# Kernel tuning notes

Hardware: AMD Instinct MI355X
Metric: run time of the kernel (lower is better)

Reference implementation:

```python
import jax, jax.numpy as jnp
import numpy as np

POS_TH = 0.5
NEG_TH = 0.4
NEGPOS_RATIO = 3
BBOX_ALPHA = 1.5
CONF_ALPHA = 1.0
VAR_CXCY = 0.1
VAR_WH = 0.2
NUM_CLASSES = 41
B, P, G = 8, 100000, 16


def setup_inputs() -> dict:
    key = jax.random.key(0)
    k = jax.random.split(key, 8)
    loc_data = jax.random.normal(k[0], (B, P, 4), dtype=jnp.float32)
    conf_data = jax.random.normal(k[1], (B, P, NUM_CLASSES), dtype=jnp.float32)
    # priors in (cx, cy, w, h), normalized coords
    p_cxy = jax.random.uniform(k[2], (P, 2), minval=0.0, maxval=1.0)
    p_wh = jax.random.uniform(k[3], (P, 2), minval=0.02, maxval=0.3)
    priors = jnp.concatenate([p_cxy, p_wh], axis=1).astype(jnp.float32)
    # gt boxes in point form (x1, y1, x2, y2)
    g_cxy = jax.random.uniform(k[4], (B, G, 2), minval=0.15, maxval=0.85)
    g_wh = jax.random.uniform(k[5], (B, G, 2), minval=0.05, maxval=0.4)
    gt_boxes = jnp.concatenate([
        jnp.clip(g_cxy - g_wh / 2, 0.0, 1.0),
        jnp.clip(g_cxy + g_wh / 2, 0.0, 1.0),
    ], axis=-1).astype(jnp.float32)
    gt_labels = jax.random.randint(k[6], (B, G), 1, NUM_CLASSES)
    return {"loc_data": loc_data, "conf_data": conf_data, "priors": priors,
            "gt_boxes": gt_boxes, "gt_labels": gt_labels}


def point_form(pr):
    return jnp.concatenate([pr[:, :2] - pr[:, 2:] / 2,
                            pr[:, :2] + pr[:, 2:] / 2], axis=1)


def jaccard(a, b):
    # a: [G,4] xyxy, b: [P,4] xyxy -> [G,P]
    lt = jnp.maximum(a[:, None, :2], b[None, :, :2])
    rb = jnp.minimum(a[:, None, 2:], b[None, :, 2:])
    wh = jnp.clip(rb - lt, 0.0)
    inter = wh[..., 0] * wh[..., 1]
    area_a = ((a[:, 2] - a[:, 0]) * (a[:, 3] - a[:, 1]))[:, None]
    area_b = ((b[:, 2] - b[:, 0]) * (b[:, 3] - b[:, 1]))[None, :]
    return inter / (area_a + area_b - inter)


def encode(matched, priors):
    # matched [P,4] xyxy, priors [P,4] cxcywh -> SSD offsets with variances
    g_cxcy = ((matched[:, :2] + matched[:, 2:]) / 2 - priors[:, :2]) / (VAR_CXCY * priors[:, 2:])
    g_wh = jnp.log(jnp.clip((matched[:, 2:] - matched[:, :2]) / priors[:, 2:], 1e-8)) / VAR_WH
    return jnp.concatenate([g_cxcy, g_wh], axis=1)


def match_one(gt_box, gt_label, priors):
    # gt_box [G,4], gt_label [G], priors [P,4] -> loc_t [P,4], conf_t [P]
    pf = point_form(priors)
    ov = jaccard(gt_box, pf)                      # [G,P]
    best_truth_ov = ov.max(axis=0)                # [P]
    best_truth_idx = ov.argmax(axis=0)            # [P]
    best_prior_idx = ov.argmax(axis=1)            # [G] best prior per gt
    # force-match each gt to its best prior
    best_truth_ov = best_truth_ov.at[best_prior_idx].set(2.0)
    best_truth_idx = best_truth_idx.at[best_prior_idx].set(jnp.arange(gt_box.shape[0]))
    conf = gt_label[best_truth_idx]
    conf = jnp.where(best_truth_ov < POS_TH, -1, conf)   # neutral
    conf = jnp.where(best_truth_ov < NEG_TH, 0, conf)    # background
    loc = encode(gt_box[best_truth_idx], priors)
    return loc, conf


def reference(loc_data, conf_data, priors, gt_boxes, gt_labels):
    bsz, n_pri, n_cls = conf_data.shape
    loc_t, conf_t = jax.vmap(match_one, in_axes=(0, 0, None))(gt_boxes, gt_labels, priors)
    pos = conf_t > 0                               # [B,P]
    num_pos = pos.sum(axis=1)                      # [B]
    # pos_weights: uniform 1/num_pos per image (ones split then normalized)
    pos_w = pos.astype(loc_data.dtype) / jnp.clip(num_pos, 1).astype(loc_data.dtype)[:, None]
    # localization: weighted SmoothL1 over positives
    d = loc_data - loc_t
    sl1 = jnp.where(jnp.abs(d) < 1.0, 0.5 * d * d, jnp.abs(d) - 0.5)
    loss_B = (pos_w[..., None] * sl1).sum() * BBOX_ALPHA
    # OHEM hard negative mining on background-suppression loss
    loss_c = jax.nn.logsumexp(conf_data, axis=-1) - conf_data[..., 0]
    loss_c = jnp.where(pos | (conf_t < 0), 0.0, loss_c)
    order = jnp.argsort(-loss_c, axis=1)
    rank = jnp.argsort(order, axis=1)
    num_neg = jnp.clip(NEGPOS_RATIO * num_pos, 0, n_pri - 1)
    neg = (rank < num_neg[:, None]) & (~pos) & (conf_t >= 0)
    keep = (pos | neg).astype(conf_data.dtype)
    logp = jax.nn.log_softmax(conf_data, axis=-1)
    ce = -jnp.take_along_axis(logp, jnp.clip(conf_t, 0)[..., None], axis=-1)[..., 0]
    total_pos = jnp.clip(num_pos.sum(), 1).astype(conf_data.dtype)
    loss_C = (ce * keep).sum() * CONF_ALPHA / total_pos
    return (loss_B + loss_C) / bsz
```

## Files before the change

kernel.cpp:

```cpp
#include <hip/hip_runtime.h>
#include <stdint.h>

#define BATCH 8
#define NPRI 100000
#define NGT 16
#define NCLS 41
#define F_POS_TH 0.5f
#define F_NEG_TH 0.4f

static constexpr int TPB = 256;
static constexpr int MCHUNK = 16;
static constexpr int MLEN = (NPRI + MCHUNK - 1) / MCHUNK;

static constexpr int WTPB = 64;
static constexpr int CPT = WTPB * NCLS / 4;
static constexpr int BLK_PER_B = 224;
static constexpr int TILES_PER_B = (NPRI + WTPB - 1) / WTPB;
static constexpr int H0BIN = 256;
static constexpr int NBIN = 4096;

static constexpr size_t OFF_KEY  = 0;
static constexpr size_t OFF_GTC  = OFF_KEY + (size_t)BATCH*NPRI*4;
static constexpr size_t OFF_HG   = OFF_GTC + BATCH*NGT*8;
static constexpr size_t OFF_NPOS = OFF_HG + (size_t)BATCH*H0BIN*4;
static constexpr size_t OFF_SL1  = OFF_NPOS + BATCH*4;
static constexpr size_t OFF_CEP  = OFF_SL1  + BATCH*4;
static constexpr size_t OFF_NEG  = OFF_CEP  + BATCH*4;
static constexpr size_t OFF_FTK  = OFF_NEG  + BATCH*4;
static constexpr int ZERO_U32 = (int)((OFF_FTK + 4 - OFF_HG) / 4);

__device__ inline float smoothl1(float d) {
  float a = fabsf(d);
  return a < 1.f ? 0.5f * d * d : a - 0.5f;
}
__device__ inline float aload_f32(const float* p) {
  return __hip_atomic_load(p, __ATOMIC_RELAXED, __HIP_MEMORY_SCOPE_AGENT);
}
__device__ __forceinline__ void gll16(const void* gsrc, void* ldst) {
  __builtin_amdgcn_global_load_lds(
      (const __attribute__((address_space(1))) void*)gsrc,
      (__attribute__((address_space(3))) void*)ldst, 16, 0, 0);
}

__global__ void k_init(unsigned* __restrict__ z, unsigned long long* __restrict__ gtc) {
  int t = threadIdx.x;
  for (int i = t; i < ZERO_U32; i += 512) z[i] = 0u;
  if (t < BATCH * NGT) gtc[t] = 0xFFFFFFFFull;
}

__global__ __launch_bounds__(TPB) void k_match(const float* __restrict__ priors,
                                               const float* __restrict__ gtb,
                                               unsigned long long* __restrict__ gtc) {
  int bg = blockIdx.y;
  int t = threadIdx.x;
  const float4 gv = ((const float4*)gtb)[bg];
  float garea = (gv.z - gv.x) * (gv.w - gv.y);
  int pend = min(NPRI, (int)(blockIdx.x + 1) * MLEN);
  unsigned long long best = 0;
  for (int p = blockIdx.x * MLEN + t; p < pend; p += TPB) {
    float4 pv = ((const float4*)priors)[p];
    float px1 = pv.x - 0.5f * pv.z, py1 = pv.y - 0.5f * pv.w;
    float px2 = pv.x + 0.5f * pv.z, py2 = pv.y + 0.5f * pv.w;
    float ix = fmaxf(fminf(px2, gv.z) - fmaxf(px1, gv.x), 0.f);
    float iy = fmaxf(fminf(py2, gv.w) - fmaxf(py1, gv.y), 0.f);
    float inter = ix * iy;
    float parea = (px2 - px1) * (py2 - py1);
    float iou = inter / (parea + garea - inter);
    unsigned long long comp = ((unsigned long long)__float_as_uint(iou) << 32)
                            | (unsigned long long)(0xFFFFFFFFu - (unsigned)p);
    best = best > comp ? best : comp;
  }
#pragma unroll
  for (int off = 32; off; off >>= 1) {
    unsigned long long o = (unsigned long long)__shfl_xor((long long)best, off, 64);
    best = best > o ? best : o;
  }
  __shared__ unsigned long long red[4];
  if ((t & 63) == 0) red[t >> 6] = best;
  __syncthreads();
  if (t == 0) {
    unsigned long long r = red[0];
    r = r > red[1] ? r : red[1];
    r = r > red[2] ? r : red[2];
    r = r > red[3] ? r : red[3];
    atomicMax(&gtc[bg], r);
  }
}

__global__ __launch_bounds__(WTPB) void k_conf(
    const float* __restrict__ loc, const float* __restrict__ conf,
    const float* __restrict__ priors, const float* __restrict__ gtb,
    const int* __restrict__ gtl, const unsigned long long* __restrict__ gtc,
    unsigned* __restrict__ key, unsigned* __restrict__ histg,
    unsigned* __restrict__ npos, float* __restrict__ sl1sum, float* __restrict__ cepos) {
  __shared__ float buf[2][CPT * 4];
  __shared__ unsigned hcb[H0BIN];
  int t = threadIdx.x;
  int b = blockIdx.x / BLK_PER_B;
  int sub = blockIdx.x % BLK_PER_B;
  const float4* conf4 = (const float4*)conf;
  const size_t bbase4 = (size_t)b * NPRI * NCLS / 4;
  const size_t maxc4 = (size_t)BATCH * NPRI * NCLS / 4 - 1;
  float acc_s = 0.f, acc_c = 0.f; unsigned acc_p = 0;
#pragma unroll
  for (int u = 0; u < H0BIN / WTPB; u++) hcb[t + u * WTPB] = 0u;

  {
    size_t base4 = bbase4 + (size_t)sub * CPT;
#pragma unroll
    for (int u = 0; u < 10; u++) {
      size_t g4 = base4 + (unsigned)(t + u * WTPB);
      if (g4 > maxc4) g4 = maxc4;
      gll16(conf4 + g4, &buf[0][(t + u * WTPB) * 4]);
    }
    if (t < CPT - 10 * WTPB) {
      size_t g4 = base4 + (unsigned)(t + 10 * WTPB);
      if (g4 > maxc4) g4 = maxc4;
      gll16(conf4 + g4, &buf[0][(t + 10 * WTPB) * 4]);
    }
  }
  int cur = 0;
  for (int tidx = sub; tidx < TILES_PER_B; tidx += BLK_PER_B) {
    int p = tidx * WTPB + t;
    bool valid = p < NPRI;
    int pc = valid ? p : NPRI - 1;
    float4 pv = ((const float4*)priors)[pc];
    float4 ld = ((const float4*)loc)[(size_t)b * NPRI + pc];
    int nxt = tidx + BLK_PER_B;
    if (nxt < TILES_PER_B) {
      size_t base4 = bbase4 + (size_t)nxt * CPT;
#pragma unroll
      for (int u = 0; u < 10; u++) {
        size_t g4 = base4 + (unsigned)(t + u * WTPB);
        if (g4 > maxc4) g4 = maxc4;
        gll16(conf4 + g4, &buf[cur ^ 1][(t + u * WTPB) * 4]);
      }
      if (t < CPT - 10 * WTPB) {
        size_t g4 = base4 + (unsigned)(t + 10 * WTPB);
        if (g4 > maxc4) g4 = maxc4;
        gll16(conf4 + g4, &buf[cur ^ 1][(t + 10 * WTPB) * 4]);
      }
      asm volatile("s_waitcnt vmcnt(11)" ::: "memory");
    } else {
      asm volatile("s_waitcnt vmcnt(0)" ::: "memory");
    }
    __builtin_amdgcn_sched_barrier(0);
    unsigned kkreg = 0u;
    if (valid) {
      float px1 = pv.x - 0.5f * pv.z, py1 = pv.y - 0.5f * pv.w;
      float px2 = pv.x + 0.5f * pv.z, py2 = pv.y + 0.5f * pv.w;
      float parea = (px2 - px1) * (py2 - py1);
      float bov = 0.f; int g = 0;
#pragma unroll
      for (int gg = 0; gg < NGT; gg++) {
        const float4 gv = ((const float4*)gtb)[b * NGT + gg];
        float ix = fmaxf(fminf(px2, gv.z) - fmaxf(px1, gv.x), 0.f);
        float iy = fmaxf(fminf(py2, gv.w) - fmaxf(py1, gv.y), 0.f);
        float inter = ix * iy;
        float garea = (gv.z - gv.x) * (gv.w - gv.y);
        float iou = inter / (parea + garea - inter);
        if (iou > bov) { bov = iou; g = gg; }
      }
      float o = bov;
#pragma unroll
      for (int gg = 0; gg < NGT; gg++) {
        unsigned long long c64 = gtc[b * NGT + gg];
        unsigned pw = 0xFFFFFFFFu - (unsigned)(c64 & 0xFFFFFFFFull);
        if ((unsigned)p == pw) { o = 2.0f; g = gg; }
      }
      int c = gtl[b * NGT + g];
      if (o < F_POS_TH) c = -1;
      if (o < F_NEG_TH) c = 0;
      const float* r = &buf[cur][t * NCLS];
      float s = 0.f, r0 = 0.f, rc = 0.f;
#pragma unroll
      for (int j = 0; j < NCLS; j++) {
        float v = r[j];
        s += __expf(v);
        if (j == 0) r0 = v;
        if (j == c) rc = v;
      }
      float lse = __logf(s);
      kkreg = (c == 0) ? __float_as_uint(lse - r0) : 0u;
      key[(size_t)b * NPRI + p] = kkreg;
      atomicAdd(&hcb[kkreg >> 24], 1u);
      if (c > 0) {
        acc_p += 1;
        acc_c += lse - rc;
        const float4 gvb = ((const float4*)gtb)[b * NGT + g];
        float tx = ((gvb.x + gvb.z) * 0.5f - pv.x) / (0.1f * pv.z);
        float ty = ((gvb.y + gvb.w) * 0.5f - pv.y) / (0.1f * pv.w);
        float tw = __logf(fmaxf((gvb.z - gvb.x) / pv.z, 1e-8f)) / 0.2f;
        float th = __logf(fmaxf((gvb.w - gvb.y) / pv.w, 1e-8f)) / 0.2f;
        acc_s += smoothl1(ld.x - tx) + smoothl1(ld.y - ty)
               + smoothl1(ld.z - tw) + smoothl1(ld.w - th);
      }
    }
    cur ^= 1;
  }
#pragma unroll
  for (int u = 0; u < H0BIN / WTPB; u++) {
    unsigned v = hcb[t + u * WTPB];
    if (v) atomicAdd(&histg[b * H0BIN + t + u * WTPB], v);
  }
  float vs = acc_s, vc = acc_c; unsigned vp = acc_p;
#pragma unroll
  for (int off = 32; off; off >>= 1) {
    vs += __shfl_down(vs, off, 64);
    vc += __shfl_down(vc, off, 64);
    vp += __shfl_down(vp, off, 64);
  }
  if (t == 0) {
    if (vp) atomicAdd(&npos[b], vp);
    if (vs != 0.f) atomicAdd(&sl1sum[b], vs);
    if (vc != 0.f) atomicAdd(&cepos[b], vc);
  }
}

__global__ __launch_bounds__(1024) void k_select(
    const unsigned* __restrict__ key, const unsigned* __restrict__ histg,
    const unsigned* __restrict__ npos, const float* __restrict__ sl1sum,
    const float* __restrict__ cepos, float* __restrict__ negsum,
    unsigned* __restrict__ final_tk, float* __restrict__ out) {
  __shared__ unsigned hc[NBIN];
  __shared__ unsigned pcs[256], sc[256];
  __shared__ int wA; __shared__ unsigned kexA;
  __shared__ unsigned kS, prefS;
  __shared__ float redf[16];
  int b = blockIdx.x, t = threadIdx.x;
  unsigned k0 = min(3u * npos[b], (unsigned)(NPRI - 1));
  const int iters = (NPRI + 1023) / 1024;
  if (t < 256) { unsigned v = histg[b * H0BIN + t]; pcs[t] = v; sc[t] = v; }
  if (t == 0) { kS = 0u; prefS = 0u; wA = -1; }
  __syncthreads();
  for (int off = 1; off < 256; off <<= 1) {
    unsigned v = 0;
    if (t < 256) v = (t + off < 256) ? sc[t + off] : 0u;
    __syncthreads();
    if (t < 256) sc[t] += v;
    __syncthreads();
  }
  if (t < 256) {
    unsigned excl = sc[t] - pcs[t];
    if (k0 > 0 && excl < k0 && k0 <= excl + pcs[t]) { wA = t; kexA = excl; }
  }
  __syncthreads();
  if (t == 0 && wA >= 0) { prefS = ((unsigned)wA) << 24; kS = k0 - kexA; }
  __syncthreads();
  for (int lvl = 1; lvl <= 2; lvl++) {
    unsigned k = kS;
    int shift = (lvl == 1) ? 12 : 0;
    int lowcut = (lvl == 1) ? 24 : 12;
    for (int i = t; i < NBIN; i += 1024) hc[i] = 0u;
    if (t == 0) wA = -1;
    __syncthreads();
    unsigned pre = prefS >> lowcut;
    if (k > 0) {
      for (int n = 0; n < iters; n++) {
        int i = n * 1024 + t;
        if (i < NPRI) {
          unsigned kk = key[(size_t)b * NPRI + i];
          if ((kk >> lowcut) == pre) atomicAdd(&hc[(kk >> shift) & 0xFFFu], 1u);
        }
      }
    }
    __syncthreads();
    if (t < 256) {
      unsigned cs = 0;
#pragma unroll
      for (int u = 0; u < 16; u++) cs += hc[t * 16 + u];
      pcs[t] = cs; sc[t] = cs;
    }
    __syncthreads();
    for (int off = 1; off < 256; off <<= 1) {
      unsigned v = 0;
      if (t < 256) v = (t + off < 256) ? sc[t + off] : 0u;
      __syncthreads();
      if (t < 256) sc[t] += v;
      __syncthreads();
    }
    if (t < 256) {
      unsigned excl = sc[t] - pcs[t];
      if (k > 0 && excl < k && k <= excl + pcs[t]) { wA = t; kexA = excl; }
    }
    __syncthreads();
    if (wA >= 0 && t < 64) {
      int w = wA; unsigned exw = kexA;
      unsigned v = (t < 16) ? hc[w * 16 + t] : 0u;
      unsigned sufv = v;
#pragma unroll
      for (int off = 1; off < 16; off <<= 1) {
        unsigned x = __shfl_down(sufv, off, 64);
        if (t + off < 16) sufv += x;
      }
      unsigned excl2 = exw + (sufv - v);
      if (t < 16 && excl2 < k && k <= excl2 + v) {
        prefS |= ((unsigned)(w * 16 + t)) << shift;
        kS = k - excl2;
      }
    }
    __syncthreads();
  }
  unsigned Tu = prefS;
  unsigned tie = kS;
  float acc = 0.f;
  if (k0 > 0) {
    for (int n = 0; n < iters; n++) {
      int i = n * 1024 + t;
      if (i < NPRI) {
        unsigned kk = key[(size_t)b * NPRI + i];
        if (kk > Tu) acc += __uint_as_float(kk);
      }
    }
  }
#pragma unroll
  for (int off = 32; off; off >>= 1) acc += __shfl_down(acc, off, 64);
  if ((t & 63) == 0) redf[t >> 6] = acc;
  __syncthreads();
  if (t == 0) {
    float tot = 0.f;
    for (int wv = 0; wv < 16; wv++) tot += redf[wv];
    if (k0 > 0) tot += (float)tie * __uint_as_float(Tu);
    negsum[b] = tot;
    __threadfence();
    unsigned r2 = atomicAdd(final_tk, 1u);
    if (r2 == BATCH - 1) {
      __threadfence();
      float lb = 0.f, ctot = 0.f; unsigned tp = 0;
      for (int bb = 0; bb < BATCH; bb++) {
        lb += aload_f32(&sl1sum[bb]) / fmaxf((float)npos[bb], 1.f);
        tp += npos[bb];
        ctot += aload_f32(&cepos[bb]) + aload_f32(&negsum[bb]);
      }
      out[0] = (1.5f * lb + ctot / fmaxf((float)tp, 1.f)) / (float)BATCH;
      *final_tk = 0;
    }
  }
}

extern "C" void kernel_launch(void* const* d_in, const int* in_sizes, int n_in,
                              void* d_out, int out_size, void* d_ws, size_t ws_size,
                              hipStream_t stream) {
  const float* loc = (const float*)d_in[0];
  const float* conf = (const float*)d_in[1];
  const float* priors = (const float*)d_in[2];
  const float* gtb = (const float*)d_in[3];
  const int* gtl = (const int*)d_in[4];
  char* ws = (char*)d_ws;
  unsigned* key = (unsigned*)(ws + OFF_KEY);
  unsigned long long* gtc = (unsigned long long*)(ws + OFF_GTC);
  unsigned* histg = (unsigned*)(ws + OFF_HG);
  unsigned* npos = (unsigned*)(ws + OFF_NPOS);
  float* sl1sum = (float*)(ws + OFF_SL1);
  float* cepos = (float*)(ws + OFF_CEP);
  float* negsum = (float*)(ws + OFF_NEG);
  unsigned* final_tk = (unsigned*)(ws + OFF_FTK);
  float* out = (float*)d_out;

  k_init<<<1, 512, 0, stream>>>(histg, gtc);
  dim3 gridM(MCHUNK, BATCH * NGT);
  k_match<<<gridM, TPB, 0, stream>>>(priors, gtb, gtc);
  k_conf<<<BATCH * BLK_PER_B, WTPB, 0, stream>>>(loc, conf, priors, gtb, gtl, gtc,
                                                 key, histg, npos, sl1sum, cepos);
  k_select<<<BATCH, 1024, 0, stream>>>(key, histg, npos, sl1sum, cepos,
                                       negsum, final_tk, out);
}
```

Measured before the change: 151.3 us.

## Replace LDS double-buffered conf loads with coalesced register loads and shared atomic row sums

The persistent 64-thread double-buffered global_load_lds pipeline in k_conf is replaced by a one-tile-per-wave grid of 256-thread blocks. Each lane loads 11 coalesced float4 chunks straight into registers, exponentiates them, and accumulates per-prior exp sums into shared memory with atomics split at row boundaries. The positive-class logit is then re-read from global memory, and per-block reductions go through shared memory. This trades the explicit prefetch pipeline for more occupancy and parallelism, at the cost of many LDS atomics and a much larger grid.

```diff
diff --git a/kernel.cpp b/kernel.cpp
--- a/kernel.cpp
+++ b/kernel.cpp
@@ -12,10 +12,9 @@
 static constexpr int MCHUNK = 16;
 static constexpr int MLEN = (NPRI + MCHUNK - 1) / MCHUNK;
 
-static constexpr int WTPB = 64;
-static constexpr int CPT = WTPB * NCLS / 4;
-static constexpr int BLK_PER_B = 224;
-static constexpr int TILES_PER_B = (NPRI + WTPB - 1) / WTPB;
+static constexpr int TILES_PER_B = (NPRI + 63) / 64;
+static constexpr int CBLK = (TILES_PER_B + 3) / 4;
+static constexpr int CW = 64 * NCLS / 4;
 static constexpr int H0BIN = 256;
 static constexpr int NBIN = 4096;
 
@@ -29,17 +28,14 @@
 static constexpr size_t OFF_FTK  = OFF_NEG  + BATCH*4;
 static constexpr int ZERO_U32 = (int)((OFF_FTK + 4 - OFF_HG) / 4);
 
+typedef float f32x4 __attribute__((ext_vector_type(4)));
+
 __device__ inline float smoothl1(float d) {
   float a = fabsf(d);
   return a < 1.f ? 0.5f * d * d : a - 0.5f;
 }
 __device__ inline float aload_f32(const float* p) {
   return __hip_atomic_load(p, __ATOMIC_RELAXED, __HIP_MEMORY_SCOPE_AGENT);
-}
-__device__ __forceinline__ void gll16(const void* gsrc, void* ldst) {
-  __builtin_amdgcn_global_load_lds(
-      (const __attribute__((address_space(1))) void*)gsrc,
-      (__attribute__((address_space(3))) void*)ldst, 16, 0, 0);
 }
 
 __global__ void k_init(unsigned* __restrict__ z, unsigned long long* __restrict__ gtc) {
@@ -53,16 +49,16 @@
                                                unsigned long long* __restrict__ gtc) {
   int bg = blockIdx.y;
   int t = threadIdx.x;
-  const float4 gv = ((const float4*)gtb)[bg];
-  float garea = (gv.z - gv.x) * (gv.w - gv.y);
+  const f32x4 gv = ((const f32x4*)gtb)[bg];
+  float garea = (gv[2] - gv[0]) * (gv[3] - gv[1]);
   int pend = min(NPRI, (int)(blockIdx.x + 1) * MLEN);
   unsigned long long best = 0;
   for (int p = blockIdx.x * MLEN + t; p < pend; p += TPB) {
-    float4 pv = ((const float4*)priors)[p];
-    float px1 = pv.x - 0.5f * pv.z, py1 = pv.y - 0.5f * pv.w;
-    float px2 = pv.x + 0.5f * pv.z, py2 = pv.y + 0.5f * pv.w;
-    float ix = fmaxf(fminf(px2, gv.z) - fmaxf(px1, gv.x), 0.f);
-    float iy = fmaxf(fminf(py2, gv.w) - fmaxf(py1, gv.y), 0.f);
+    f32x4 pv = ((const f32x4*)priors)[p];
+    float px1 = pv[0] - 0.5f * pv[2], py1 = pv[1] - 0.5f * pv[3];
+    float px2 = pv[0] + 0.5f * pv[2], py2 = pv[1] + 0.5f * pv[3];
+    float ix = fmaxf(fminf(px2, gv[2]) - fmaxf(px1, gv[0]), 0.f);
+    float iy = fmaxf(fminf(py2, gv[3]) - fmaxf(py1, gv[1]), 0.f);
     float inter = ix * iy;
     float parea = (px2 - px1) * (py2 - py1);
     float iou = inter / (parea + garea - inter);
@@ -87,77 +83,78 @@
   }
 }
 
-__global__ __launch_bounds__(WTPB) void k_conf(
+__global__ __launch_bounds__(256, 4) void k_conf(
     const float* __restrict__ loc, const float* __restrict__ conf,
     const float* __restrict__ priors, const float* __restrict__ gtb,
     const int* __restrict__ gtl, const unsigned long long* __restrict__ gtc,
     unsigned* __restrict__ key, unsigned* __restrict__ histg,
     unsigned* __restrict__ npos, float* __restrict__ sl1sum, float* __restrict__ cepos) {
-  __shared__ float buf[2][CPT * 4];
+  __shared__ float sums[4][64];
+  __shared__ float r0s[4][64];
   __shared__ unsigned hcb[H0BIN];
-  int t = threadIdx.x;
-  int b = blockIdx.x / BLK_PER_B;
-  int sub = blockIdx.x % BLK_PER_B;
-  const float4* conf4 = (const float4*)conf;
-  const size_t bbase4 = (size_t)b * NPRI * NCLS / 4;
-  const size_t maxc4 = (size_t)BATCH * NPRI * NCLS / 4 - 1;
-  float acc_s = 0.f, acc_c = 0.f; unsigned acc_p = 0;
-#pragma unroll
-  for (int u = 0; u < H0BIN / WTPB; u++) hcb[t + u * WTPB] = 0u;
-
-  {
-    size_t base4 = bbase4 + (size_t)sub * CPT;
-#pragma unroll
-    for (int u = 0; u < 10; u++) {
-      size_t g4 = base4 + (unsigned)(t + u * WTPB);
-      if (g4 > maxc4) g4 = maxc4;
-      gll16(conf4 + g4, &buf[0][(t + u * WTPB) * 4]);
-    }
-    if (t < CPT - 10 * WTPB) {
-      size_t g4 = base4 + (unsigned)(t + 10 * WTPB);
-      if (g4 > maxc4) g4 = maxc4;
-      gll16(conf4 + g4, &buf[0][(t + 10 * WTPB) * 4]);
-    }
-  }
-  int cur = 0;
-  for (int tidx = sub; tidx < TILES_PER_B; tidx += BLK_PER_B) {
-    int p = tidx * WTPB + t;
-    bool valid = p < NPRI;
-    int pc = valid ? p : NPRI - 1;
-    float4 pv = ((const float4*)priors)[pc];
-    float4 ld = ((const float4*)loc)[(size_t)b * NPRI + pc];
-    int nxt = tidx + BLK_PER_B;
-    if (nxt < TILES_PER_B) {
-      size_t base4 = bbase4 + (size_t)nxt * CPT;
-#pragma unroll
-      for (int u = 0; u < 10; u++) {
-        size_t g4 = base4 + (unsigned)(t + u * WTPB);
-        if (g4 > maxc4) g4 = maxc4;
-        gll16(conf4 + g4, &buf[cur ^ 1][(t + u * WTPB) * 4]);
-      }
-      if (t < CPT - 10 * WTPB) {
-        size_t g4 = base4 + (unsigned)(t + 10 * WTPB);
-        if (g4 > maxc4) g4 = maxc4;
-        gll16(conf4 + g4, &buf[cur ^ 1][(t + 10 * WTPB) * 4]);
-      }
-      asm volatile("s_waitcnt vmcnt(11)" ::: "memory");
-    } else {
-      asm volatile("s_waitcnt vmcnt(0)" ::: "memory");
-    }
-    __builtin_amdgcn_sched_barrier(0);
-    unsigned kkreg = 0u;
+  __shared__ float redS[4], redC[4]; __shared__ unsigned redP[4];
+  const int t = threadIdx.x, w = t >> 6, l = t & 63;
+  const int b = blockIdx.y;
+  const int tile = blockIdx.x * 4 + w;
+  hcb[t] = 0u;
+  sums[w][l] = 0.f;
+  __syncthreads();
+  float accS = 0.f, accC = 0.f; unsigned accP = 0;
+  if (tile < TILES_PER_B) {
+    const f32x4* c4 = (const f32x4*)conf;
+    const size_t base = (size_t)b * (NPRI * NCLS / 4) + (size_t)tile * CW;
+    const size_t bend = (size_t)(b + 1) * (NPRI * NCLS / 4) - 1;
+    f32x4 rr[11];
+#pragma unroll
+    for (int u = 0; u < 11; u++) {
+      size_t ix = base + (unsigned)(u * 64 + l);
+      if (ix > bend) ix = bend;
+      rr[u] = c4[ix];
+    }
+    const int p = tile * 64 + l;
+    const bool valid = p < NPRI;
+    const int pc = valid ? p : NPRI - 1;
+    const f32x4 pv = ((const f32x4*)priors)[pc];
+    const f32x4 ld = ((const f32x4*)loc)[(size_t)b * NPRI + pc];
+#pragma unroll
+    for (int u = 0; u < 11; u++) {
+      int cidx = u * 64 + l;
+      if (cidx < CW) {
+        int f = cidx * 4;
+        int r0 = (int)((unsigned)f / 41u);
+        int rem = f - r0 * 41;
+        float e0 = __expf(rr[u][0]);
+        float e1 = __expf(rr[u][1]);
+        float e2 = __expf(rr[u][2]);
+        float e3 = __expf(rr[u][3]);
+        int nlo = 41 - rem;
+        float slo = e0, shi = 0.f;
+        if (nlo > 1) slo += e1; else shi += e1;
+        if (nlo > 2) slo += e2; else shi += e2;
+        if (nlo > 3) slo += e3; else shi += e3;
+        atomicAdd(&sums[w][r0], slo);
+        if (nlo <= 3) atomicAdd(&sums[w][r0 + 1], shi);
+        if (rem == 0) r0s[w][r0] = rr[u][0];
+        else if (nlo <= 3) {
+          float v = (nlo == 1) ? rr[u][1] : (nlo == 2) ? rr[u][2] : rr[u][3];
+          r0s[w][r0 + 1] = v;
+        }
+      }
+    }
+    float lse = __logf(sums[w][l]);
+    float r0v = r0s[w][l];
     if (valid) {
-      float px1 = pv.x - 0.5f * pv.z, py1 = pv.y - 0.5f * pv.w;
-      float px2 = pv.x + 0.5f * pv.z, py2 = pv.y + 0.5f * pv.w;
+      float px1 = pv[0] - 0.5f * pv[2], py1 = pv[1] - 0.5f * pv[3];
+      float px2 = pv[0] + 0.5f * pv[2], py2 = pv[1] + 0.5f * pv[3];
       float parea = (px2 - px1) * (py2 - py1);
       float bov = 0.f; int g = 0;
 #pragma unroll
       for (int gg = 0; gg < NGT; gg++) {
-        const float4 gv = ((const float4*)gtb)[b * NGT + gg];
-        float ix = fmaxf(fminf(px2, gv.z) - fmaxf(px1, gv.x), 0.f);
-        float iy = fmaxf(fminf(py2, gv.w) - fmaxf(py1, gv.y), 0.f);
+        const f32x4 gv = ((const f32x4*)gtb)[b * NGT + gg];
+        float ix = fmaxf(fminf(px2, gv[2]) - fmaxf(px1, gv[0]), 0.f);
+        float iy = fmaxf(fminf(py2, gv[3]) - fmaxf(py1, gv[1]), 0.f);
         float inter = ix * iy;
-        float garea = (gv.z - gv.x) * (gv.w - gv.y);
+        float garea = (gv[2] - gv[0]) * (gv[3] - gv[1]);
         float iou = inter / (parea + garea - inter);
         if (iou > bov) { bov = iou; g = gg; }
       }
@@ -171,49 +168,41 @@
       int c = gtl[b * NGT + g];
       if (o < F_POS_TH) c = -1;
       if (o < F_NEG_TH) c = 0;
-      const float* r = &buf[cur][t * NCLS];
-      float s = 0.f, r0 = 0.f, rc = 0.f;
-#pragma unroll
-      for (int j = 0; j < NCLS; j++) {
-        float v = r[j];
-        s += __expf(v);
-        if (j == 0) r0 = v;
-        if (j == c) rc = v;
-      }
-      float lse = __logf(s);
-      kkreg = (c == 0) ? __float_as_uint(lse - r0) : 0u;
+      unsigned kkreg = (c == 0) ? __float_as_uint(lse - r0v) : 0u;
       key[(size_t)b * NPRI + p] = kkreg;
       atomicAdd(&hcb[kkreg >> 24], 1u);
       if (c > 0) {
-        acc_p += 1;
-        acc_c += lse - rc;
-        const float4 gvb = ((const float4*)gtb)[b * NGT + g];
-        float tx = ((gvb.x + gvb.z) * 0.5f - pv.x) / (0.1f * pv.z);
-        float ty = ((gvb.y + gvb.w) * 0.5f - pv.y) / (0.1f * pv.w);
-        float tw = __logf(fmaxf((gvb.z - gvb.x) / pv.z, 1e-8f)) / 0.2f;
-        float th = __logf(fmaxf((gvb.w - gvb.y) / pv.w, 1e-8f)) / 0.2f;
-        acc_s += smoothl1(ld.x - tx) + smoothl1(ld.y - ty)
-               + smoothl1(ld.z - tw) + smoothl1(ld.w - th);
-      }
-    }
-    cur ^= 1;
-  }
-#pragma unroll
-  for (int u = 0; u < H0BIN / WTPB; u++) {
-    unsigned v = hcb[t + u * WTPB];
-    if (v) atomicAdd(&histg[b * H0BIN + t + u * WTPB], v);
-  }
-  float vs = acc_s, vc = acc_c; unsigned vp = acc_p;
+        accP = 1;
+        float rc = conf[((size_t)b * NPRI + p) * NCLS + c];
+        accC = lse - rc;
+        const f32x4 gvb = ((const f32x4*)gtb)[b * NGT + g];
+        float tx = ((gvb[0] + gvb[2]) * 0.5f - pv[0]) / (0.1f * pv[2]);
+        float ty = ((gvb[1] + gvb[3]) * 0.5f - pv[1]) / (0.1f * pv[3]);
+        float tw = __logf(fmaxf((gvb[2] - gvb[0]) / pv[2], 1e-8f)) / 0.2f;
+        float th = __logf(fmaxf((gvb[3] - gvb[1]) / pv[3], 1e-8f)) / 0.2f;
+        accS = smoothl1(ld[0] - tx) + smoothl1(ld[1] - ty)
+             + smoothl1(ld[2] - tw) + smoothl1(ld[3] - th);
+      }
+    }
+  }
+  __syncthreads();
+  { unsigned v = hcb[t]; if (v) atomicAdd(&histg[b * H0BIN + t], v); }
+  float vs = accS, vc = accC; unsigned vp = accP;
 #pragma unroll
   for (int off = 32; off; off >>= 1) {
     vs += __shfl_down(vs, off, 64);
     vc += __shfl_down(vc, off, 64);
     vp += __shfl_down(vp, off, 64);
   }
+  if (l == 0) { redS[w] = vs; redC[w] = vc; redP[w] = vp; }
+  __syncthreads();
   if (t == 0) {
-    if (vp) atomicAdd(&npos[b], vp);
-    if (vs != 0.f) atomicAdd(&sl1sum[b], vs);
-    if (vc != 0.f) atomicAdd(&cepos[b], vc);
+    float ts = redS[0] + redS[1] + redS[2] + redS[3];
+    float tc = redC[0] + redC[1] + redC[2] + redC[3];
+    unsigned tp = redP[0] + redP[1] + redP[2] + redP[3];
+    if (tp) atomicAdd(&npos[b], tp);
+    if (ts != 0.f) atomicAdd(&sl1sum[b], ts);
+    if (tc != 0.f) atomicAdd(&cepos[b], tc);
   }
 }
 
@@ -360,8 +349,9 @@
   k_init<<<1, 512, 0, stream>>>(histg, gtc);
   dim3 gridM(MCHUNK, BATCH * NGT);
   k_match<<<gridM, TPB, 0, stream>>>(priors, gtb, gtc);
-  k_conf<<<BATCH * BLK_PER_B, WTPB, 0, stream>>>(loc, conf, priors, gtb, gtl, gtc,
-                                                 key, histg, npos, sl1sum, cepos);
+  dim3 gridC(CBLK, BATCH);
+  k_conf<<<gridC, 256, 0, stream>>>(loc, conf, priors, gtb, gtl, gtc,
+                                    key, histg, npos, sl1sum, cepos);
   k_select<<<BATCH, 1024, 0, stream>>>(key, histg, npos, sl1sum, cepos,
                                        negsum, final_tk, out);
 }
```

Result: slower. 187.0 us (+23.6%).

## Fuse best-prior matching into conf pass and patch forced matches in select

Applied to the files above, without the earlier changes.

Removes the separate k_match kernel. The per-GT best-prior argmax is now computed inside k_conf through LDS atomicMax on packed (iou, index) keys, then merged globally. Because the forced assignment is only known after k_conf finishes, k_select corrects the 16 forced priors per image afterwards: it adjusts the key, the histogram, npos, the SmoothL1 sum and the positive CE sum. It also replaces the most common per-thread histogram atomics (zero keys and bin 0x40) with wave-ballot aggregated adds. The cost is a serial correction step in thread 0, extra LDS atomics in the hot loop, and delicate logic for duplicate forced matches.

```diff
diff --git a/kernel.cpp b/kernel.cpp
--- a/kernel.cpp
+++ b/kernel.cpp
@@ -7,10 +7,6 @@
 #define NCLS 41
 #define F_POS_TH 0.5f
 #define F_NEG_TH 0.4f
-
-static constexpr int TPB = 256;
-static constexpr int MCHUNK = 16;
-static constexpr int MLEN = (NPRI + MCHUNK - 1) / MCHUNK;
 
 static constexpr int WTPB = 64;
 static constexpr int CPT = WTPB * NCLS / 4;
@@ -29,11 +25,24 @@
 static constexpr size_t OFF_FTK  = OFF_NEG  + BATCH*4;
 static constexpr int ZERO_U32 = (int)((OFF_FTK + 4 - OFF_HG) / 4);
 
+typedef float f32x4 __attribute__((ext_vector_type(4)));
+
 __device__ inline float smoothl1(float d) {
   float a = fabsf(d);
   return a < 1.f ? 0.5f * d * d : a - 0.5f;
 }
+__device__ inline float sl1_terms(f32x4 pv, f32x4 ld, f32x4 gv) {
+  float tx = ((gv[0] + gv[2]) * 0.5f - pv[0]) / (0.1f * pv[2]);
+  float ty = ((gv[1] + gv[3]) * 0.5f - pv[1]) / (0.1f * pv[3]);
+  float tw = __logf(fmaxf((gv[2] - gv[0]) / pv[2], 1e-8f)) / 0.2f;
+  float th = __logf(fmaxf((gv[3] - gv[1]) / pv[3], 1e-8f)) / 0.2f;
+  return smoothl1(ld[0] - tx) + smoothl1(ld[1] - ty)
+       + smoothl1(ld[2] - tw) + smoothl1(ld[3] - th);
+}
 __device__ inline float aload_f32(const float* p) {
+  return __hip_atomic_load(p, __ATOMIC_RELAXED, __HIP_MEMORY_SCOPE_AGENT);
+}
+__device__ inline unsigned aload_u32(const unsigned* p) {
   return __hip_atomic_load(p, __ATOMIC_RELAXED, __HIP_MEMORY_SCOPE_AGENT);
 }
 __device__ __forceinline__ void gll16(const void* gsrc, void* ldst) {
@@ -48,62 +57,26 @@
   if (t < BATCH * NGT) gtc[t] = 0xFFFFFFFFull;
 }
 
-__global__ __launch_bounds__(TPB) void k_match(const float* __restrict__ priors,
-                                               const float* __restrict__ gtb,
-                                               unsigned long long* __restrict__ gtc) {
-  int bg = blockIdx.y;
-  int t = threadIdx.x;
-  const float4 gv = ((const float4*)gtb)[bg];
-  float garea = (gv.z - gv.x) * (gv.w - gv.y);
-  int pend = min(NPRI, (int)(blockIdx.x + 1) * MLEN);
-  unsigned long long best = 0;
-  for (int p = blockIdx.x * MLEN + t; p < pend; p += TPB) {
-    float4 pv = ((const float4*)priors)[p];
-    float px1 = pv.x - 0.5f * pv.z, py1 = pv.y - 0.5f * pv.w;
-    float px2 = pv.x + 0.5f * pv.z, py2 = pv.y + 0.5f * pv.w;
-    float ix = fmaxf(fminf(px2, gv.z) - fmaxf(px1, gv.x), 0.f);
-    float iy = fmaxf(fminf(py2, gv.w) - fmaxf(py1, gv.y), 0.f);
-    float inter = ix * iy;
-    float parea = (px2 - px1) * (py2 - py1);
-    float iou = inter / (parea + garea - inter);
-    unsigned long long comp = ((unsigned long long)__float_as_uint(iou) << 32)
-                            | (unsigned long long)(0xFFFFFFFFu - (unsigned)p);
-    best = best > comp ? best : comp;
-  }
-#pragma unroll
-  for (int off = 32; off; off >>= 1) {
-    unsigned long long o = (unsigned long long)__shfl_xor((long long)best, off, 64);
-    best = best > o ? best : o;
-  }
-  __shared__ unsigned long long red[4];
-  if ((t & 63) == 0) red[t >> 6] = best;
-  __syncthreads();
-  if (t == 0) {
-    unsigned long long r = red[0];
-    r = r > red[1] ? r : red[1];
-    r = r > red[2] ? r : red[2];
-    r = r > red[3] ? r : red[3];
-    atomicMax(&gtc[bg], r);
-  }
-}
-
 __global__ __launch_bounds__(WTPB) void k_conf(
     const float* __restrict__ loc, const float* __restrict__ conf,
     const float* __restrict__ priors, const float* __restrict__ gtb,
-    const int* __restrict__ gtl, const unsigned long long* __restrict__ gtc,
+    const int* __restrict__ gtl,
     unsigned* __restrict__ key, unsigned* __restrict__ histg,
+    unsigned long long* __restrict__ gtc,
     unsigned* __restrict__ npos, float* __restrict__ sl1sum, float* __restrict__ cepos) {
   __shared__ float buf[2][CPT * 4];
   __shared__ unsigned hcb[H0BIN];
+  __shared__ unsigned long long best[NGT];
   int t = threadIdx.x;
   int b = blockIdx.x / BLK_PER_B;
   int sub = blockIdx.x % BLK_PER_B;
-  const float4* conf4 = (const float4*)conf;
+  const f32x4* conf4 = (const f32x4*)conf;
   const size_t bbase4 = (size_t)b * NPRI * NCLS / 4;
   const size_t maxc4 = (size_t)BATCH * NPRI * NCLS / 4 - 1;
   float acc_s = 0.f, acc_c = 0.f; unsigned acc_p = 0;
 #pragma unroll
   for (int u = 0; u < H0BIN / WTPB; u++) hcb[t + u * WTPB] = 0u;
+  if (t < NGT) best[t] = 0;
 
   {
     size_t base4 = bbase4 + (size_t)sub * CPT;
@@ -124,8 +97,8 @@
     int p = tidx * WTPB + t;
     bool valid = p < NPRI;
     int pc = valid ? p : NPRI - 1;
-    float4 pv = ((const float4*)priors)[pc];
-    float4 ld = ((const float4*)loc)[(size_t)b * NPRI + pc];
+    f32x4 pv = ((const f32x4*)priors)[pc];
+    f32x4 ld = ((const f32x4*)loc)[(size_t)b * NPRI + pc];
     int nxt = tidx + BLK_PER_B;
     if (nxt < TILES_PER_B) {
       size_t base4 = bbase4 + (size_t)nxt * CPT;
@@ -147,30 +120,28 @@
     __builtin_amdgcn_sched_barrier(0);
     unsigned kkreg = 0u;
     if (valid) {
-      float px1 = pv.x - 0.5f * pv.z, py1 = pv.y - 0.5f * pv.w;
-      float px2 = pv.x + 0.5f * pv.z, py2 = pv.y + 0.5f * pv.w;
+      float px1 = pv[0] - 0.5f * pv[2], py1 = pv[1] - 0.5f * pv[3];
+      float px2 = pv[0] + 0.5f * pv[2], py2 = pv[1] + 0.5f * pv[3];
       float parea = (px2 - px1) * (py2 - py1);
       float bov = 0.f; int g = 0;
 #pragma unroll
       for (int gg = 0; gg < NGT; gg++) {
-        const float4 gv = ((const float4*)gtb)[b * NGT + gg];
-        float ix = fmaxf(fminf(px2, gv.z) - fmaxf(px1, gv.x), 0.f);
-        float iy = fmaxf(fminf(py2, gv.w) - fmaxf(py1, gv.y), 0.f);
+        const f32x4 gv = ((const f32x4*)gtb)[b * NGT + gg];
+        float ix = fmaxf(fminf(px2, gv[2]) - fmaxf(px1, gv[0]), 0.f);
+        float iy = fmaxf(fminf(py2, gv[3]) - fmaxf(py1, gv[1]), 0.f);
         float inter = ix * iy;
-        float garea = (gv.z - gv.x) * (gv.w - gv.y);
+        float garea = (gv[2] - gv[0]) * (gv[3] - gv[1]);
         float iou = inter / (parea + garea - inter);
         if (iou > bov) { bov = iou; g = gg; }
-      }
-      float o = bov;
-#pragma unroll
-      for (int gg = 0; gg < NGT; gg++) {
-        unsigned long long c64 = gtc[b * NGT + gg];
-        unsigned pw = 0xFFFFFFFFu - (unsigned)(c64 & 0xFFFFFFFFull);
-        if ((unsigned)p == pw) { o = 2.0f; g = gg; }
+        if (iou > 0.f) {
+          unsigned long long comp = ((unsigned long long)__float_as_uint(iou) << 32)
+                                  | (unsigned long long)(0xFFFFFFFFu - (unsigned)p);
+          if (comp > best[gg]) atomicMax(&best[gg], comp);
+        }
       }
       int c = gtl[b * NGT + g];
-      if (o < F_POS_TH) c = -1;
-      if (o < F_NEG_TH) c = 0;
+      if (bov < F_POS_TH) c = -1;
+      if (bov < F_NEG_TH) c = 0;
       const float* r = &buf[cur][t * NCLS];
       float s = 0.f, r0 = 0.f, rc = 0.f;
 #pragma unroll
@@ -183,21 +154,24 @@
       float lse = __logf(s);
       kkreg = (c == 0) ? __float_as_uint(lse - r0) : 0u;
       key[(size_t)b * NPRI + p] = kkreg;
-      atomicAdd(&hcb[kkreg >> 24], 1u);
       if (c > 0) {
         acc_p += 1;
         acc_c += lse - rc;
-        const float4 gvb = ((const float4*)gtb)[b * NGT + g];
-        float tx = ((gvb.x + gvb.z) * 0.5f - pv.x) / (0.1f * pv.z);
-        float ty = ((gvb.y + gvb.w) * 0.5f - pv.y) / (0.1f * pv.w);
-        float tw = __logf(fmaxf((gvb.z - gvb.x) / pv.z, 1e-8f)) / 0.2f;
-        float th = __logf(fmaxf((gvb.w - gvb.y) / pv.w, 1e-8f)) / 0.2f;
-        acc_s += smoothl1(ld.x - tx) + smoothl1(ld.y - ty)
-               + smoothl1(ld.z - tw) + smoothl1(ld.w - th);
-      }
-    }
+        const f32x4 gvb = ((const f32x4*)gtb)[b * NGT + g];
+        acc_s += sl1_terms(pv, ld, gvb);
+      }
+    }
+    unsigned bin = kkreg >> 24;
+    unsigned long long m40 = __ballot(valid && kkreg != 0u && bin == 0x40u);
+    unsigned long long m00 = __ballot(valid && kkreg == 0u);
+    if (m40 && t == __ffsll((long long)m40) - 1)
+      atomicAdd(&hcb[0x40], (unsigned)__popcll(m40));
+    if (m00 && t == __ffsll((long long)m00) - 1)
+      atomicAdd(&hcb[0], (unsigned)__popcll(m00));
+    if (valid && kkreg != 0u && bin != 0x40u) atomicAdd(&hcb[bin], 1u);
     cur ^= 1;
   }
+  if (t < NGT && best[t] != 0) atomicMax(&gtc[b * NGT + t], best[t]);
 #pragma unroll
   for (int u = 0; u < H0BIN / WTPB; u++) {
     unsigned v = hcb[t + u * WTPB];
@@ -218,20 +192,86 @@
 }
 
 __global__ __launch_bounds__(1024) void k_select(
-    const unsigned* __restrict__ key, const unsigned* __restrict__ histg,
-    const unsigned* __restrict__ npos, const float* __restrict__ sl1sum,
-    const float* __restrict__ cepos, float* __restrict__ negsum,
+    const float* __restrict__ loc, const float* __restrict__ conf,
+    const float* __restrict__ priors, const float* __restrict__ gtb,
+    const int* __restrict__ gtl, const unsigned long long* __restrict__ gtc,
+    unsigned* __restrict__ key, const unsigned* __restrict__ histg,
+    unsigned* __restrict__ npos, float* __restrict__ sl1sum,
+    float* __restrict__ cepos, float* __restrict__ negsum,
     unsigned* __restrict__ final_tk, float* __restrict__ out) {
   __shared__ unsigned hc[NBIN];
+  __shared__ unsigned h0s[H0BIN];
   __shared__ unsigned pcs[256], sc[256];
   __shared__ int wA; __shared__ unsigned kexA;
   __shared__ unsigned kS, prefS;
   __shared__ float redf[16];
+  __shared__ unsigned pw16[NGT]; __shared__ float lse16[NGT], bov16[NGT];
+  __shared__ int bidx16[NGT];
   int b = blockIdx.x, t = threadIdx.x;
+  if (t < H0BIN) h0s[t] = histg[b * H0BIN + t];
+  if (t < NGT) {
+    unsigned long long c64 = gtc[b * NGT + t];
+    unsigned p = 0xFFFFFFFFu - (unsigned)(c64 & 0xFFFFFFFFull);
+    pw16[t] = p;
+    const float* row = conf + ((size_t)b * NPRI + p) * NCLS;
+    float s = 0.f;
+    for (int j = 0; j < NCLS; j++) s += __expf(row[j]);
+    lse16[t] = __logf(s);
+    f32x4 pv = ((const f32x4*)priors)[p];
+    float px1 = pv[0] - 0.5f * pv[2], py1 = pv[1] - 0.5f * pv[3];
+    float px2 = pv[0] + 0.5f * pv[2], py2 = pv[1] + 0.5f * pv[3];
+    float parea = (px2 - px1) * (py2 - py1);
+    float bov = 0.f; int g = 0;
+    for (int gg = 0; gg < NGT; gg++) {
+      const f32x4 gv = ((const f32x4*)gtb)[b * NGT + gg];
+      float ix = fmaxf(fminf(px2, gv[2]) - fmaxf(px1, gv[0]), 0.f);
+      float iy = fmaxf(fminf(py2, gv[3]) - fmaxf(py1, gv[1]), 0.f);
+      float inter = ix * iy;
+      float garea = (gv[2] - gv[0]) * (gv[3] - gv[1]);
+      float iou = inter / (parea + garea - inter);
+      if (iou > bov) { bov = iou; g = gg; }
+    }
+    bov16[t] = bov; bidx16[t] = g;
+  }
+  __syncthreads();
+  if (t == 0) {
+    unsigned np = npos[b];
+    float sl = sl1sum[b], cpv = cepos[b];
+    for (int i = 0; i < NGT; i++) {
+      unsigned p = pw16[i];
+      int prev = -1;
+      for (int j = 0; j < i; j++) if (pw16[j] == p) prev = j;
+      float lse = lse16[i];
+      const float* row = conf + ((size_t)b * NPRI + p) * NCLS;
+      f32x4 pv = ((const f32x4*)priors)[p];
+      f32x4 ldv = ((const f32x4*)loc)[(size_t)b * NPRI + p];
+      float newce = lse - row[gtl[b * NGT + i]];
+      float newsl = sl1_terms(pv, ldv, ((const f32x4*)gtb)[b * NGT + i]);
+      if (prev < 0) {
+        float o = bov16[i]; int gold = bidx16[i];
+        int cold = (o < F_NEG_TH) ? 0 : ((o < F_POS_TH) ? -1 : gtl[b * NGT + gold]);
+        if (cold == 0) {
+          unsigned ko = key[(size_t)b * NPRI + p];
+          h0s[ko >> 24] -= 1u; h0s[0] += 1u;
+        } else if (cold > 0) {
+          np -= 1; cpv -= lse - row[cold];
+          sl -= sl1_terms(pv, ldv, ((const f32x4*)gtb)[b * NGT + gold]);
+        }
+        np += 1; cpv += newce; sl += newsl;
+        key[(size_t)b * NPRI + p] = 0u;
+      } else {
+        cpv -= lse - row[gtl[b * NGT + prev]];
+        sl -= sl1_terms(pv, ldv, ((const f32x4*)gtb)[b * NGT + prev]);
+        cpv += newce; sl += newsl;
+      }
+    }
+    npos[b] = np; sl1sum[b] = sl; cepos[b] = cpv;
+    kS = 0u; prefS = 0u; wA = -1;
+  }
+  __syncthreads();
   unsigned k0 = min(3u * npos[b], (unsigned)(NPRI - 1));
   const int iters = (NPRI + 1023) / 1024;
-  if (t < 256) { unsigned v = histg[b * H0BIN + t]; pcs[t] = v; sc[t] = v; }
-  if (t == 0) { kS = 0u; prefS = 0u; wA = -1; }
+  if (t < 256) { unsigned v = h0s[t]; pcs[t] = v; sc[t] = v; }
   __syncthreads();
   for (int off = 1; off < 256; off <<= 1) {
     unsigned v = 0;
@@ -328,8 +368,9 @@
       __threadfence();
       float lb = 0.f, ctot = 0.f; unsigned tp = 0;
       for (int bb = 0; bb < BATCH; bb++) {
-        lb += aload_f32(&sl1sum[bb]) / fmaxf((float)npos[bb], 1.f);
-        tp += npos[bb];
+        unsigned nb = aload_u32(&npos[bb]);
+        lb += aload_f32(&sl1sum[bb]) / fmaxf((float)nb, 1.f);
+        tp += nb;
         ctot += aload_f32(&cepos[bb]) + aload_f32(&negsum[bb]);
       }
       out[0] = (1.5f * lb + ctot / fmaxf((float)tp, 1.f)) / (float)BATCH;
@@ -358,10 +399,9 @@
   float* out = (float*)d_out;
 
   k_init<<<1, 512, 0, stream>>>(histg, gtc);
-  dim3 gridM(MCHUNK, BATCH * NGT);
-  k_match<<<gridM, TPB, 0, stream>>>(priors, gtb, gtc);
-  k_conf<<<BATCH * BLK_PER_B, WTPB, 0, stream>>>(loc, conf, priors, gtb, gtl, gtc,
-                                                 key, histg, npos, sl1sum, cepos);
-  k_select<<<BATCH, 1024, 0, stream>>>(key, histg, npos, sl1sum, cepos,
+  k_conf<<<BATCH * BLK_PER_B, WTPB, 0, stream>>>(loc, conf, priors, gtb, gtl,
+                                                 key, histg, gtc, npos, sl1sum, cepos);
+  k_select<<<BATCH, 1024, 0, stream>>>(loc, conf, priors, gtb, gtl, gtc,
+                                       key, histg, npos, sl1sum, cepos,
                                        negsum, final_tk, out);
 }
```

New measurement: 178.2 us. 1.18x slower.
